# Kernel optimization log

Measured on AMD Instinct MI355X. Metric: run time of the kernel, lower is better.

Reference implementation:

```python
import jax, jax.numpy as jnp
import numpy as np

B, M, GRID = 4, 8192, 32          # batches, points per batch, voxel grid side
N = B * M
K = 8                              # knn neighbors (includes self at dist 0)
C_IN, C_OUT, H = 8, 8, 128
KEYB = 64                          # hash base (coords shifted +1 stay in [0,33])
EPS = 1e-5


def setup_inputs() -> dict:
    rng = np.random.default_rng(0)
    # unique occupied voxels per batch (ME SparseTensor requires unique coords)
    cs = []
    for b in range(B):
        lin = rng.choice(GRID ** 3, size=M, replace=False)
        x, y, z = lin // (GRID * GRID), (lin // GRID) % GRID, lin % GRID
        cs.append(np.stack([np.full(M, b), x, y, z], axis=1))
    coords = jnp.asarray(np.concatenate(cs, axis=0).astype(np.int32))  # [N,4]

    key = jax.random.key(0)
    ks = jax.random.split(key, 4)
    feats = jax.random.normal(ks[0], (N, C_IN), jnp.float32)
    w1 = jax.random.normal(ks[1], ((K + 1) * C_IN, H), jnp.float32) * 0.05  # 1x1 conv
    g1 = jnp.ones((H,), jnp.float32)
    b1 = jnp.zeros((H,), jnp.float32)
    w3 = jax.random.normal(ks[2], (27, H, H), jnp.float32) * 0.02          # 3^3 sparse conv
    g2 = jnp.ones((H,), jnp.float32)
    b2 = jnp.zeros((H,), jnp.float32)
    w_out = jax.random.normal(ks[3], (H, 2 * C_OUT), jnp.float32) * 0.05   # 1x1 conv
    return dict(coords=coords, feats=feats, w1=w1, g1=g1, b1=b1,
                w3=w3, g2=g2, b2=b2, w_out=w_out)


def _knn_idx(coords):
    # per-batch brute-force kNN on xyz (batch column segments the search)
    xyz = coords[:, 1:].astype(jnp.float32).reshape(B, M, 3)
    d2 = jnp.sum((xyz[:, :, None, :] - xyz[:, None, :, :]) ** 2, -1)  # [B,M,M]
    _, idx = jax.lax.top_k(-d2, K)                                     # [B,M,K]
    return (idx + (jnp.arange(B) * M)[:, None, None]).reshape(N, K)


def _bn(x, g, b):
    mu = jnp.mean(x, axis=0)
    var = jnp.var(x, axis=0)
    return (x - mu) * jax.lax.rsqrt(var + EPS) * g + b


def reference(coords, feats, w1, g1, b1, w3, g2, b2, w_out):
    # --- kNN gather-and-build: [center || k neighbor feats] -> (k+1)*C_in ---
    nbr = _knn_idx(coords)                                        # [N,K] int
    combined = jnp.concatenate([feats[:, None, :], feats[nbr]], axis=1)
    combined = combined.reshape(N, (K + 1) * C_IN)
    # --- neighbor_processor: 1x1 conv + BN + ReLU ---
    h = jax.nn.relu(_bn(combined @ w1, g1, b1))                   # [N,H]
    # --- context_predictor conv k=3: gather inputs at coord+offset via hash ---
    c = coords[:, 1:] + 1                                         # shift so offsets stay >= 0
    keys = ((coords[:, 0] * KEYB + c[:, 0]) * KEYB + c[:, 1]) * KEYB + c[:, 2]
    order = jnp.argsort(keys)
    skeys = keys[order]
    offs = jnp.stack(jnp.meshgrid(*([jnp.arange(-1, 2)] * 3), indexing='ij'),
                     axis=-1).reshape(27, 3)                      # {-1,0,1}^3
    okey = (offs[:, 0] * KEYB + offs[:, 1]) * KEYB + offs[:, 2]   # [27]
    q = keys[None, :] + okey[:, None]                             # [27,N]
    pos = jnp.clip(jnp.searchsorted(skeys, q), 0, N - 1)
    valid = skeys[pos] == q                                       # [27,N]
    j = order[pos]                                                # [27,N]
    gathered = jnp.where(valid[..., None], h[j], 0.0)             # [27,N,H]
    h2 = jnp.einsum('onc,ocd->nd', gathered, w3)                  # [N,H]
    h2 = jax.nn.relu(_bn(h2, g2, b2))
    # --- final 1x1 conv -> mean/scale ---
    return h2 @ w_out                                             # [N, 2*C_OUT]
```

## Files before the change

kernel.cpp:

```cpp
#include <hip/hip_runtime.h>
#include <hip/hip_bf16.h>

#define B_   4
#define M_   8192
#define N_   32768
#define H_   128
#define EPS_ 1e-5f
#define TBL  1048576
#define GUARD 8192

typedef short short8 __attribute__((ext_vector_type(8)));
typedef float f32x4  __attribute__((ext_vector_type(4)));

__global__ __launch_bounds__(256) void prep_kernel(const int* __restrict__ coords,
                                                   int* __restrict__ table,
                                                   int* __restrict__ packed,
                                                   int* __restrict__ keyb,
                                                   float* __restrict__ gsum,
                                                   unsigned int* __restrict__ hbz) {
    int n = blockIdx.x * 256 + threadIdx.x;
    int b = coords[4*n+0], x = coords[4*n+1], y = coords[4*n+2], z = coords[4*n+3];
    packed[n] = (x << 10) | (y << 5) | z;
    int key = ((b*64 + x+1)*64 + y+1)*64 + (z+1);
    keyb[n] = key;
    table[key] = n;
    if (blockIdx.x == 0) gsum[threadIdx.x] = 0.f;
    if (blockIdx.x == 1 && threadIdx.x < 64) hbz[threadIdx.x] = 0u;
}

__global__ __launch_bounds__(256) void w3pack_kernel(const float* __restrict__ w3,
                                                     ushort* __restrict__ w3f) {
    int t = blockIdx.x * 256 + threadIdx.x;
    int lane = t & 63;
    int ct   = (t >> 6) & 7;
    int ks   = (t >> 9) & 3;
    int o    = t >> 11;
    int quad = lane >> 4, l15 = lane & 15;
    int n = ct*16 + l15;
    const float* src = w3 + o*16384;
    ushort out8[8];
#pragma unroll
    for (int j = 0; j < 8; ++j) {
        int c = ks*32 + quad*8 + j;
        float v = src[c*128 + n];
        __hip_bfloat16 bv = __float2bfloat16(v);
        ushort u; __builtin_memcpy(&u, &bv, 2);
        out8[j] = u;
    }
    *(uint4*)&w3f[t*8] = *(uint4*)out8;
}

__global__ __launch_bounds__(256) void knn_window_kernel(const int* __restrict__ table,
                                                         const int* __restrict__ keyb,
                                                         int* __restrict__ nbr,
                                                         int* __restrict__ flagcnt,
                                                         int* __restrict__ flaglist) {
    __shared__ int okey_sh[125], d2_sh[125];
    __shared__ int tops[256 * 8];
    int tid = threadIdx.x;
    if (tid < 125) {
        int dx = tid / 25 - 2, rr = tid % 25, dy = rr / 5 - 2, dz = rr % 5 - 2;
        okey_sh[tid] = dx * 4096 + dy * 64 + dz;
        d2_sh[tid]   = dx*dx + dy*dy + dz*dz;
    }
    __syncthreads();

    int q   = blockIdx.x * 64 + (tid >> 2);
    int sub = tid & 3;
    int kb  = keyb[q];

    int top[8];
#pragma unroll
    for (int k = 0; k < 8; ++k) top[k] = 0x7FFFFFFF;

    int base = sub * 32;
    int cnt  = (sub == 3) ? 29 : 32;
    for (int i = 0; i < cnt; ++i) {
        int idx = base + i;
        int j = table[kb + okey_sh[idx]];
        if (j >= 0) {
            int key = (d2_sh[idx] << 13) | (j & 8191);
            if (key < top[7]) {
#pragma unroll
                for (int k = 7; k >= 1; --k)
                    top[k] = (key < top[k]) ? max(key, top[k-1]) : top[k];
                top[0] = min(key, top[0]);
            }
        }
    }
#pragma unroll
    for (int k = 0; k < 8; ++k) tops[tid*8 + k] = top[k];
    __syncthreads();

    if (sub == 0) {
        const int* L = &tops[tid*8];
        int ia0 = 0, ia1 = 0, ia2 = 0, ia3 = 0;
        int res[8];
#pragma unroll
        for (int k = 0; k < 8; ++k) {
            int v0 = L[ia0], v1 = L[8 + ia1], v2 = L[16 + ia2], v3 = L[24 + ia3];
            int m01 = min(v0, v1), m23 = min(v2, v3);
            int m = min(m01, m23);
            res[k] = m;
            if (m == v0) ++ia0; else if (m == v1) ++ia1;
            else if (m == v2) ++ia2; else ++ia3;
        }
        int bb = q & ~(M_-1);
        if ((res[7] >> 13) <= 8) {
#pragma unroll
            for (int k = 0; k < 8; ++k) nbr[q*8 + k] = bb + (res[k] & 8191);
        } else {
            int pos = atomicAdd(flagcnt, 1);
            flaglist[pos] = q;
        }
    }
}

__global__ __launch_bounds__(256) void knn_bf_kernel(const int* __restrict__ packed,
                                                     const int* __restrict__ flagcnt,
                                                     const int* __restrict__ flaglist,
                                                     int* __restrict__ nbr) {
    __shared__ int tops[256 * 8];
    int tid = threadIdx.x;
    int cnt = *flagcnt;
    for (int f = blockIdx.x; f < cnt; f += gridDim.x) {
        int n = flaglist[f];
        int bb = n & ~(M_-1);
        int p = packed[n];
        int qx = (p >> 10) & 31, qy = (p >> 5) & 31, qz = p & 31;
        int top[8];
#pragma unroll
        for (int k = 0; k < 8; ++k) top[k] = 0x7FFFFFFF;
        for (int j = tid; j < M_; j += 256) {
            int c = packed[bb + j];
            int dx = qx - ((c >> 10) & 31);
            int dy = qy - ((c >> 5) & 31);
            int dz = qz - (c & 31);
            int d2 = dx*dx + dy*dy + dz*dz;
            int key = (d2 << 13) | j;
            if (key < top[7]) {
#pragma unroll
                for (int k = 7; k >= 1; --k)
                    top[k] = (key < top[k]) ? max(key, top[k-1]) : top[k];
                top[0] = min(key, top[0]);
            }
        }
#pragma unroll
        for (int k = 0; k < 8; ++k) tops[tid*8 + k] = top[k];
        __syncthreads();
        for (int stride = 128; stride >= 1; stride >>= 1) {
            if (tid < stride) {
                int* A  = &tops[tid*8];
                int* Bp = &tops[(tid+stride)*8];
                int r[8]; int ia = 0, ib = 0;
#pragma unroll
                for (int k = 0; k < 8; ++k) {
                    int a = A[ia], b2 = Bp[ib];
                    if (a <= b2) { r[k] = a; ++ia; } else { r[k] = b2; ++ib; }
                }
#pragma unroll
                for (int k = 0; k < 8; ++k) A[k] = r[k];
            }
            __syncthreads();
        }
        if (tid == 0) {
#pragma unroll
            for (int k = 0; k < 8; ++k) nbr[n*8 + k] = bb + (tops[k] & 8191);
        }
        __syncthreads();
    }
}

__global__ __launch_bounds__(256) void h1_kernel(const float* __restrict__ feats,
                                                 const int* __restrict__ nbr,
                                                 const float* __restrict__ w1,
                                                 float* __restrict__ hpre) {
    __shared__ float comb[16][72];
    int tid = threadIdx.x;
    int rowbase = blockIdx.x * 16;
    if (tid < 144) {
        int r = tid / 9, s = tid % 9;
        int grow = rowbase + r;
        int idx = (s == 0) ? grow : nbr[grow*8 + (s-1)];
        const float4* f = (const float4*)(feats + idx * 8);
        float4 a = f[0], b = f[1];
        float* dp = &comb[r][s*8];
        dp[0]=a.x; dp[1]=a.y; dp[2]=a.z; dp[3]=a.w;
        dp[4]=b.x; dp[5]=b.y; dp[6]=b.z; dp[7]=b.w;
    }
    __syncthreads();
    int c = tid & 127, rh = tid >> 7;
    float acc[8];
#pragma unroll
    for (int i = 0; i < 8; ++i) acc[i] = 0.f;
    for (int s = 0; s < 72; ++s) {
        float w = w1[s*128 + c];
#pragma unroll
        for (int i = 0; i < 8; ++i)
            acc[i] += comb[rh*8 + i][s] * w;
    }
#pragma unroll
    for (int i = 0; i < 8; ++i)
        hpre[(rowbase + rh*8 + i)*128 + c] = acc[i];
}

__global__ __launch_bounds__(256) void reduce_kernel(const float* __restrict__ src,
                                                     float* __restrict__ part) {
    __shared__ float ssum[256], ssq[256];
    int tid = threadIdx.x;
    int c = tid & 127, halfr = tid >> 7;
    int rowbase = blockIdx.x * 128 + halfr * 64;
    float s = 0.f, q = 0.f;
    for (int i = 0; i < 64; ++i) {
        float v = src[(rowbase + i)*128 + c];
        s += v; q += v*v;
    }
    ssum[tid] = s; ssq[tid] = q;
    __syncthreads();
    if (tid < 128) {
        part[blockIdx.x*256 + tid]       = ssum[tid] + ssum[tid+128];
        part[blockIdx.x*256 + 128 + tid] = ssq[tid]  + ssq[tid+128];
    }
}

__global__ __launch_bounds__(128) void stats_kernel(const float* __restrict__ part,
                                                    const float* __restrict__ g,
                                                    const float* __restrict__ bias,
                                                    float* __restrict__ scale,
                                                    float* __restrict__ shift) {
    int c = threadIdx.x;
    float s = 0.f, q = 0.f;
    for (int b = 0; b < 256; ++b) {
        s += part[b*256 + c];
        q += part[b*256 + 128 + c];
    }
    float mu  = s / (float)N_;
    float var = q / (float)N_ - mu*mu;
    float inv = rsqrtf(var + EPS_);
    float sc  = inv * g[c];
    scale[c] = sc;
    shift[c] = bias[c] - mu * sc;
}

__global__ __launch_bounds__(128) void stats2_kernel(const float* __restrict__ gsum,
                                                     const float* __restrict__ g,
                                                     const float* __restrict__ bias,
                                                     float* __restrict__ scale,
                                                     float* __restrict__ shift) {
    int c = threadIdx.x;
    float s = gsum[c], q = gsum[128 + c];
    float mu  = s / (float)N_;
    float var = q / (float)N_ - mu*mu;
    float inv = rsqrtf(var + EPS_);
    float sc  = inv * g[c];
    scale[c] = sc;
    shift[c] = bias[c] - mu * sc;
}

__global__ __launch_bounds__(256) void bnrelu_bf16_kernel(const float* __restrict__ x,
                                                          const float* __restrict__ scale,
                                                          const float* __restrict__ shift,
                                                          ushort* __restrict__ y) {
    int i = blockIdx.x * 256 + threadIdx.x;
    float4 v = ((const float4*)x)[i];
    int c = (i * 4) & 127;
    v.x = fmaxf(0.f, v.x*scale[c]   + shift[c]);
    v.y = fmaxf(0.f, v.y*scale[c+1] + shift[c+1]);
    v.z = fmaxf(0.f, v.z*scale[c+2] + shift[c+2]);
    v.w = fmaxf(0.f, v.w*scale[c+3] + shift[c+3]);
    ushort o[4];
#pragma unroll
    for (int k = 0; k < 4; ++k) {
        float f = (&v.x)[k];
        __hip_bfloat16 bv = __float2bfloat16(f);
        __builtin_memcpy(&o[k], &bv, 2);
    }
    ((ushort4*)y)[i] = make_ushort4(o[0], o[1], o[2], o[3]);
}

#define CONV3_LDS 145408
__global__ __launch_bounds__(512) void conv3_mfma_kernel(const ushort* __restrict__ hb,
                                                         const ushort* __restrict__ w3f,
                                                         const int* __restrict__ table,
                                                         const int* __restrict__ keyb,
                                                         float* __restrict__ h2,
                                                         float* __restrict__ gsum) {
    extern __shared__ char smem_raw[];
    ushort* Asb = (ushort*)smem_raw;
    ushort* Bsb = (ushort*)(smem_raw + 65536);
    int*    jsh = (int*)(smem_raw + 131072);
    int*    kbsh= (int*)(smem_raw + 144896);

    int tid = threadIdx.x;
    int lane = tid & 63, wid = tid >> 6;
    int quad = lane >> 4, l15 = lane & 15;
    int bid = blockIdx.x;
    int swz = (bid & 7) * 32 + (bid >> 3);
    int rowbase = swz * 128;
    int wr = wid >> 1;
    int cb = (wid & 1) * 4;

    if (tid < 128) kbsh[tid] = keyb[rowbase + tid];
    __syncthreads();
    for (int t = tid; t < 27*128; t += 512) {
        int o = t >> 7, r = t & 127;
        int dx = o/9 - 1, dy = (o/3)%3 - 1, dz = o%3 - 1;
        jsh[t] = table[kbsh[r] + dx*4096 + dy*64 + dz];
    }
    __syncthreads();

#pragma unroll
    for (int i = 0; i < 4; ++i) {
        int flat = i*512 + tid;
        int r = flat >> 4, cp = flat & 15;
        int j = jsh[r];
        const ushort* asrc = hb + j*128 + ((cp ^ (r & 15)) << 3);
        __builtin_amdgcn_global_load_lds(
            (const __attribute__((address_space(1))) unsigned int*)asrc,
            (__attribute__((address_space(3))) unsigned int*)&Asb[flat << 3],
            16, 0, 0);
        __builtin_amdgcn_global_load_lds(
            (const __attribute__((address_space(1))) unsigned int*)(w3f + (flat << 3)),
            (__attribute__((address_space(3))) unsigned int*)&Bsb[flat << 3],
            16, 0, 0);
    }
    __syncthreads();

    f32x4 acc[2][4];
#pragma unroll
    for (int i = 0; i < 2; ++i)
#pragma unroll
        for (int c = 0; c < 4; ++c)
            acc[i][c] = (f32x4){0.f, 0.f, 0.f, 0.f};

    int cur = 0;
#pragma unroll 1
    for (int o = 0; o < 27; ++o) {
        if (o < 26) {
            int obase = (o + 1) << 7;
            const ushort* wsrc = w3f + ((o + 1) << 14);
            int dst = (cur ^ 1) * 16384;
#pragma unroll
            for (int i = 0; i < 4; ++i) {
                int flat = i*512 + tid;
                int r = flat >> 4, cp = flat & 15;
                int j = jsh[obase + r];
                const ushort* asrc = hb + j*128 + ((cp ^ (r & 15)) << 3);
                __builtin_amdgcn_global_load_lds(
                    (const __attribute__((address_space(1))) unsigned int*)asrc,
                    (__attribute__((address_space(3))) unsigned int*)&Asb[dst + (flat << 3)],
                    16, 0, 0);
                __builtin_amdgcn_global_load_lds(
                    (const __attribute__((address_space(1))) unsigned int*)(wsrc + (flat << 3)),
                    (__attribute__((address_space(3))) unsigned int*)&Bsb[dst + (flat << 3)],
                    16, 0, 0);
            }
        }
        const ushort* Ac = Asb + cur*16384;
        const ushort* Bc = Bsb + cur*16384;
#pragma unroll
        for (int ks = 0; ks < 4; ++ks) {
            short8 af[2], bfr[4];
#pragma unroll
            for (int i = 0; i < 2; ++i) {
                int lr = wr*32 + i*16 + l15;
                int chunk = (ks*4 + quad) ^ l15;
                af[i] = *(const short8*)&Ac[lr*128 + chunk*8];
            }
#pragma unroll
            for (int c = 0; c < 4; ++c)
                bfr[c] = *(const short8*)&Bc[((ks*8 + cb + c)*64 + lane) << 3];
#pragma unroll
            for (int i = 0; i < 2; ++i)
#pragma unroll
                for (int c = 0; c < 4; ++c)
                    acc[i][c] = __builtin_amdgcn_mfma_f32_16x16x32_bf16(af[i], bfr[c], acc[i][c], 0, 0, 0);
        }
        __syncthreads();
        cur ^= 1;
    }

    float s[4], q[4];
#pragma unroll
    for (int c = 0; c < 4; ++c) { s[c] = 0.f; q[c] = 0.f; }
#pragma unroll
    for (int i = 0; i < 2; ++i)
#pragma unroll
        for (int c = 0; c < 4; ++c)
#pragma unroll
            for (int r = 0; r < 4; ++r) {
                int row = rowbase + wr*32 + i*16 + quad*4 + r;
                int col = (cb + c)*16 + l15;
                float v = acc[i][c][r];
                h2[row*128 + col] = v;
                s[c] += v; q[c] += v*v;
            }
    float* red = (float*)smem_raw;
    if (tid < 256) red[tid] = 0.f;
    __syncthreads();
#pragma unroll
    for (int c = 0; c < 4; ++c) {
        int col = (cb + c)*16 + l15;
        atomicAdd(&red[col], s[c]);
        atomicAdd(&red[128 + col], q[c]);
    }
    __syncthreads();
    if (tid < 256) atomicAdd(&gsum[tid], red[tid]);
}

__global__ __launch_bounds__(256) void out_kernel(const float* __restrict__ h2,
                                                  const float* __restrict__ wout,
                                                  const float* __restrict__ scale,
                                                  const float* __restrict__ shift,
                                                  float* __restrict__ out) {
    __shared__ float sc[128], sh[128];
    int tid = threadIdx.x;
    if (tid < 128) { sc[tid] = scale[tid]; sh[tid] = shift[tid]; }
    __syncthreads();
    int r = tid >> 4, d = tid & 15;
    int row = blockIdx.x * 16 + r;
    float acc = 0.f;
    for (int c = 0; c < 128; ++c) {
        float hv = fmaxf(0.f, fmaf(h2[row*128 + c], sc[c], sh[c]));
        acc = fmaf(hv, wout[c*16 + d], acc);
    }
    out[row*16 + d] = acc;
}

extern "C" void kernel_launch(void* const* d_in, const int* in_sizes, int n_in,
                              void* d_out, int out_size, void* d_ws, size_t ws_size,
                              hipStream_t stream) {
    const int*   coords = (const int*)d_in[0];
    const float* feats  = (const float*)d_in[1];
    const float* w1     = (const float*)d_in[2];
    const float* g1     = (const float*)d_in[3];
    const float* b1     = (const float*)d_in[4];
    const float* w3     = (const float*)d_in[5];
    const float* g2     = (const float*)d_in[6];
    const float* b2     = (const float*)d_in[7];
    const float* wout   = (const float*)d_in[8];
    float* out = (float*)d_out;

    char* ws = (char*)d_ws;
    int*    table_base = (int*)(ws);
    int*    table   = table_base + GUARD;
    int*    packed  = (int*)(ws + (4352u<<10));
    int*    keyb    = (int*)(ws + (4608u<<10));
    int*    nbr     = (int*)(ws + (4864u<<10));
    int*    flagcnt = (int*)(ws + (5888u<<10));
    int*    flaglist= (int*)(ws + (5892u<<10));
    float*  part    = (float*)(ws + (6144u<<10));
    float*  scale1  = (float*)(ws + (6400u<<10));
    float*  shift1  = scale1 + 128;
    float*  scale2  = shift1 + 128;
    float*  shift2  = scale2 + 128;
    float*  gsum    = (float*)(ws + (6416u<<10));
    ushort* w3f     = (ushort*)(ws + (6656u<<10));
    ushort* hb      = (ushort*)(ws + (7680u<<10));
    float*  h       = (float*)(ws + (15872u<<10));
    float*  h2      = h;

    static bool conv3_attr_set = false;
    if (!conv3_attr_set) {
        hipFuncSetAttribute(reinterpret_cast<const void*>(&conv3_mfma_kernel),
                            hipFuncAttributeMaxDynamicSharedMemorySize, CONV3_LDS);
        conv3_attr_set = true;
    }

    hipMemsetAsync(table_base, 0xFF, (TBL + GUARD) * sizeof(int), stream);
    hipMemsetAsync(flagcnt, 0, sizeof(int), stream);
    prep_kernel      <<<N_/256, 256, 0, stream>>>(coords, table, packed, keyb,
                                                  gsum, (unsigned int*)(hb - 128));
    w3pack_kernel    <<<216, 256, 0, stream>>>(w3, w3f);
    knn_window_kernel<<<N_/64, 256, 0, stream>>>(table, keyb, nbr, flagcnt, flaglist);
    knn_bf_kernel    <<<256, 256, 0, stream>>>(packed, flagcnt, flaglist, nbr);
    h1_kernel        <<<N_/16, 256, 0, stream>>>(feats, nbr, w1, h);
    reduce_kernel    <<<N_/128, 256, 0, stream>>>(h, part);
    stats_kernel     <<<1, 128, 0, stream>>>(part, g1, b1, scale1, shift1);
    bnrelu_bf16_kernel<<<(N_*H_/4)/256, 256, 0, stream>>>(h, scale1, shift1, hb);
    conv3_mfma_kernel<<<N_/128, 512, CONV3_LDS, stream>>>(hb, w3f, table, keyb, h2, gsum);
    stats2_kernel    <<<1, 128, 0, stream>>>(gsum, g2, b2, scale2, shift2);
    out_kernel       <<<N_/16, 256, 0, stream>>>(h2, wout, scale2, shift2, out);
}
```

Before: 228.4 us.

## Triple-buffer gathered rows in conv3 and prefetch hash lookups into registers

The sparse 3x3x3 conv kernel no longer builds a neighbor-index table in LDS during a serial prologue. Each thread now keeps its row keys in registers and looks up the hash table for the offset two steps ahead. Gathered activation tiles are triple-buffered and weight tiles double-buffered. The per-offset __syncthreads is replaced by a partial vmcnt wait plus a barrier, so two offsets of loads can be in flight behind the MFMA work. This raises LDS use, adds some redundant clamped loads at the tail, and depends on hand-counted outstanding-load accounting being correct.

```diff
diff --git a/kernel.cpp b/kernel.cpp
--- a/kernel.cpp
+++ b/kernel.cpp
@@ -278,7 +278,16 @@
     ((ushort4*)y)[i] = make_ushort4(o[0], o[1], o[2], o[3]);
 }
 
-#define CONV3_LDS 145408
+#define CONV3_LDS 163840
+#define GLL(src, dst) __builtin_amdgcn_global_load_lds( \
+    (const __attribute__((address_space(1))) unsigned int*)(src), \
+    (__attribute__((address_space(3))) unsigned int*)(dst), 16, 0, 0)
+
+__device__ __forceinline__ int okey_of(int o) {
+    int dx = o/9 - 1, dy = (o/3)%3 - 1, dz = o%3 - 1;
+    return dx*4096 + dy*64 + dz;
+}
+
 __global__ __launch_bounds__(512) void conv3_mfma_kernel(const ushort* __restrict__ hb,
                                                          const ushort* __restrict__ w3f,
                                                          const int* __restrict__ table,
@@ -286,11 +295,6 @@
                                                          float* __restrict__ h2,
                                                          float* __restrict__ gsum) {
     extern __shared__ char smem_raw[];
-    ushort* Asb = (ushort*)smem_raw;
-    ushort* Bsb = (ushort*)(smem_raw + 65536);
-    int*    jsh = (int*)(smem_raw + 131072);
-    int*    kbsh= (int*)(smem_raw + 144896);
-
     int tid = threadIdx.x;
     int lane = tid & 63, wid = tid >> 6;
     int quad = lane >> 4, l15 = lane & 15;
@@ -300,31 +304,31 @@
     int wr = wid >> 1;
     int cb = (wid & 1) * 4;
 
-    if (tid < 128) kbsh[tid] = keyb[rowbase + tid];
-    __syncthreads();
-    for (int t = tid; t < 27*128; t += 512) {
-        int o = t >> 7, r = t & 127;
-        int dx = o/9 - 1, dy = (o/3)%3 - 1, dz = o%3 - 1;
-        jsh[t] = table[kbsh[r] + dx*4096 + dy*64 + dz];
-    }
-    __syncthreads();
-
+    int r0 = tid >> 4;
+    int swzoff = ((tid & 15) ^ (r0 & 15)) << 3;
+    int kb0 = keyb[rowbase + r0];
+    int kb1 = keyb[rowbase + r0 + 32];
+    int kb2 = keyb[rowbase + r0 + 64];
+    int kb3 = keyb[rowbase + r0 + 96];
+
+    int ok0 = okey_of(0), ok1 = okey_of(1), ok2 = okey_of(2);
+    int j00 = table[kb0+ok0], j01 = table[kb1+ok0], j02 = table[kb2+ok0], j03 = table[kb3+ok0];
+    int j10 = table[kb0+ok1], j11 = table[kb1+ok1], j12 = table[kb2+ok1], j13 = table[kb3+ok1];
+    int jc0 = table[kb0+ok2], jc1 = table[kb1+ok2], jc2 = table[kb2+ok2], jc3 = table[kb3+ok2];
+
+    GLL(hb + j00*128 + swzoff, smem_raw + 0     + ((0*512+tid) << 4));
+    GLL(hb + j01*128 + swzoff, smem_raw + 0     + ((1*512+tid) << 4));
+    GLL(hb + j02*128 + swzoff, smem_raw + 0     + ((2*512+tid) << 4));
+    GLL(hb + j03*128 + swzoff, smem_raw + 0     + ((3*512+tid) << 4));
 #pragma unroll
     for (int i = 0; i < 4; ++i) {
         int flat = i*512 + tid;
-        int r = flat >> 4, cp = flat & 15;
-        int j = jsh[r];
-        const ushort* asrc = hb + j*128 + ((cp ^ (r & 15)) << 3);
-        __builtin_amdgcn_global_load_lds(
-            (const __attribute__((address_space(1))) unsigned int*)asrc,
-            (__attribute__((address_space(3))) unsigned int*)&Asb[flat << 3],
-            16, 0, 0);
-        __builtin_amdgcn_global_load_lds(
-            (const __attribute__((address_space(1))) unsigned int*)(w3f + (flat << 3)),
-            (__attribute__((address_space(3))) unsigned int*)&Bsb[flat << 3],
-            16, 0, 0);
-    }
-    __syncthreads();
+        GLL(w3f + flat*8, smem_raw + 98304 + (flat << 4));
+    }
+    GLL(hb + j10*128 + swzoff, smem_raw + 32768 + ((0*512+tid) << 4));
+    GLL(hb + j11*128 + swzoff, smem_raw + 32768 + ((1*512+tid) << 4));
+    GLL(hb + j12*128 + swzoff, smem_raw + 32768 + ((2*512+tid) << 4));
+    GLL(hb + j13*128 + swzoff, smem_raw + 32768 + ((3*512+tid) << 4));
 
     f32x4 acc[2][4];
 #pragma unroll
@@ -333,31 +337,32 @@
         for (int c = 0; c < 4; ++c)
             acc[i][c] = (f32x4){0.f, 0.f, 0.f, 0.f};
 
-    int cur = 0;
+    int aRd = 0, aNx = 32768, aW = 65536;
+    int bRd = 98304, bW = 131072;
+
 #pragma unroll 1
     for (int o = 0; o < 27; ++o) {
-        if (o < 26) {
-            int obase = (o + 1) << 7;
-            const ushort* wsrc = w3f + ((o + 1) << 14);
-            int dst = (cur ^ 1) * 16384;
-#pragma unroll
-            for (int i = 0; i < 4; ++i) {
-                int flat = i*512 + tid;
-                int r = flat >> 4, cp = flat & 15;
-                int j = jsh[obase + r];
-                const ushort* asrc = hb + j*128 + ((cp ^ (r & 15)) << 3);
-                __builtin_amdgcn_global_load_lds(
-                    (const __attribute__((address_space(1))) unsigned int*)asrc,
-                    (__attribute__((address_space(3))) unsigned int*)&Asb[dst + (flat << 3)],
-                    16, 0, 0);
-                __builtin_amdgcn_global_load_lds(
-                    (const __attribute__((address_space(1))) unsigned int*)(wsrc + (flat << 3)),
-                    (__attribute__((address_space(3))) unsigned int*)&Bsb[dst + (flat << 3)],
-                    16, 0, 0);
-            }
-        }
-        const ushort* Ac = Asb + cur*16384;
-        const ushort* Bc = Bsb + cur*16384;
+        asm volatile("s_waitcnt vmcnt(4)" ::: "memory");
+        __builtin_amdgcn_s_barrier();
+
+        int on = (o+3 < 27) ? o+3 : 26;
+        int okn = okey_of(on);
+        int jn0 = table[kb0+okn], jn1 = table[kb1+okn], jn2 = table[kb2+okn], jn3 = table[kb3+okn];
+
+        int ob = (o+1 < 27) ? o+1 : 26;
+        const ushort* wsrc = w3f + (ob << 14);
+#pragma unroll
+        for (int i = 0; i < 4; ++i) {
+            int flat = i*512 + tid;
+            GLL(wsrc + flat*8, smem_raw + bW + (flat << 4));
+        }
+        GLL(hb + jc0*128 + swzoff, smem_raw + aW + ((0*512+tid) << 4));
+        GLL(hb + jc1*128 + swzoff, smem_raw + aW + ((1*512+tid) << 4));
+        GLL(hb + jc2*128 + swzoff, smem_raw + aW + ((2*512+tid) << 4));
+        GLL(hb + jc3*128 + swzoff, smem_raw + aW + ((3*512+tid) << 4));
+
+        const ushort* Ac = (const ushort*)(smem_raw + aRd);
+        const ushort* Bc = (const ushort*)(smem_raw + bRd);
 #pragma unroll
         for (int ks = 0; ks < 4; ++ks) {
             short8 af[2], bfr[4];
@@ -376,9 +381,13 @@
                 for (int c = 0; c < 4; ++c)
                     acc[i][c] = __builtin_amdgcn_mfma_f32_16x16x32_bf16(af[i], bfr[c], acc[i][c], 0, 0, 0);
         }
-        __syncthreads();
-        cur ^= 1;
-    }
+
+        jc0 = jn0; jc1 = jn1; jc2 = jn2; jc3 = jn3;
+        int t = aRd; aRd = aNx; aNx = aW; aW = t;
+        t = bRd; bRd = bW; bW = t;
+    }
+
+    __syncthreads();
 
     float s[4], q[4];
 #pragma unroll
```

Measured after the change: 227.3 us. No clear change (-0.5%).
